# Kernel tuning notes

Hardware: AMD Instinct MI355X
Metric: run time of the kernel (lower is better)

Reference implementation:

```python
import jax, jax.numpy as jnp
import numpy as np
import math

B, C, H, W, P = 8, 64, 256, 256, 16


def _conv2d(x, w, groups=1):
    # x: [B,C,H,W], w: [O, I/groups, kh, kw], 'SAME' padding, stride 1
    return jax.lax.conv_general_dilated(
        x, w, window_strides=(1, 1), padding='SAME',
        dimension_numbers=('NCHW', 'OIHW', 'NCHW'),
        feature_group_count=groups)


def _bn(x, g, b, m, v, eps=1e-5):
    # inference-mode BatchNorm2d over channel dim
    inv = jax.lax.rsqrt(v + eps)
    return (x - m[None, :, None, None]) * (g * inv)[None, :, None, None] + b[None, :, None, None]


def _layernorm(x, g, b, eps=1e-5):
    mu = x.mean(-1, keepdims=True)
    var = ((x - mu) ** 2).mean(-1, keepdims=True)
    return (x - mu) * jax.lax.rsqrt(var + eps) * g + b


def setup_inputs() -> dict:
    key = jax.random.key(0)
    ks = jax.random.split(key, 16)
    feat_map = jax.random.normal(ks[0], (B, C, H, W), jnp.float32)
    query = jax.random.normal(ks[1], (B, P, C), jnp.float32)
    key_tokens = jax.random.normal(ks[2], (B, H * W, C), jnp.float32)
    s = 1.0 / math.sqrt(C)
    dw_w = jax.random.normal(ks[3], (C, 1, 3, 3), jnp.float32) * (1.0 / 3.0)
    pw_w = jax.random.normal(ks[4], (C, C, 1, 1), jnp.float32) * s
    bn1_g = jnp.ones((C,)); bn1_b = jnp.zeros((C,))
    bn1_m = jnp.zeros((C,)); bn1_v = jnp.ones((C,))
    bn2_g = jnp.ones((C,)); bn2_b = jnp.zeros((C,))
    bn2_m = jnp.zeros((C,)); bn2_v = jnp.ones((C,))
    aff_w = jax.random.normal(ks[5], (P, C), jnp.float32) * s
    loc_w1 = jax.random.normal(ks[6], (C, C), jnp.float32) * s
    loc_b1 = jnp.zeros((C,))
    loc_w2 = jax.random.normal(ks[7], (C, C), jnp.float32) * s
    loc_b2 = jnp.zeros((C,))
    glb_w1 = jax.random.normal(ks[8], (C, C), jnp.float32) * s
    glb_b1 = jnp.zeros((C,))
    glb_w2 = jax.random.normal(ks[9], (C, C), jnp.float32) * s
    glb_b2 = jnp.zeros((C,))
    ln_g = jnp.ones((C,)); ln_b = jnp.zeros((C,))
    topo_scale = jnp.float32(0.01)
    orient_scale = jnp.float32(0.01)
    angles = jnp.linspace(0.0, math.pi, P + 1)[:-1]
    proto_orient = jnp.stack([jnp.cos(2.0 * angles), jnp.sin(2.0 * angles)], axis=1).astype(jnp.float32)
    return dict(feat_map=feat_map, query=query, key_tokens=key_tokens,
                dw_w=dw_w, bn1_g=bn1_g, bn1_b=bn1_b, bn1_m=bn1_m, bn1_v=bn1_v,
                pw_w=pw_w, bn2_g=bn2_g, bn2_b=bn2_b, bn2_m=bn2_m, bn2_v=bn2_v,
                aff_w=aff_w,
                loc_w1=loc_w1, loc_b1=loc_b1, loc_w2=loc_w2, loc_b2=loc_b2,
                glb_w1=glb_w1, glb_b1=glb_b1, glb_w2=glb_w2, glb_b2=glb_b2,
                ln_g=ln_g, ln_b=ln_b, topo_scale=topo_scale, orient_scale=orient_scale,
                proto_orient=proto_orient)


def reference(feat_map, query, key_tokens,
              dw_w, bn1_g, bn1_b, bn1_m, bn1_v,
              pw_w, bn2_g, bn2_b, bn2_m, bn2_v,
              aff_w,
              loc_w1, loc_b1, loc_w2, loc_b2,
              glb_w1, glb_b1, glb_w2, glb_b2,
              ln_g, ln_b, topo_scale, orient_scale, proto_orient):
    b, c, h, w = feat_map.shape
    hw = h * w
    # conv_spatial: depthwise 3x3 -> BN -> ReLU -> 1x1 -> BN -> ReLU
    x = _conv2d(feat_map, dw_w, groups=c)
    x = jax.nn.relu(_bn(x, bn1_g, bn1_b, bn1_m, bn1_v))
    x = _conv2d(x, pw_w)
    x = jax.nn.relu(_bn(x, bn2_g, bn2_b, bn2_m, bn2_v))
    feat_conv = x.reshape(b, c, hw).transpose(0, 2, 1)  # [B, L, C]
    # Sobel edge magnitude on channel-mean map
    edge_input = feat_map.mean(axis=1, keepdims=True)  # [B,1,H,W]
    sob_x = jnp.array([[-1, 0, 1], [-2, 0, 2], [-1, 0, 1]], jnp.float32).reshape(1, 1, 3, 3)
    sob_y = jnp.array([[-1, -2, -1], [0, 0, 0], [1, 2, 1]], jnp.float32).reshape(1, 1, 3, 3)
    gx = _conv2d(edge_input, sob_x)
    gy = _conv2d(edge_input, sob_y)
    edge_strength = jnp.sqrt(gx * gx + gy * gy + 1e-6)  # [B,1,H,W]
    # standardized edge weight over tokens (unbiased std, matching torch.std)
    ew = edge_strength.reshape(b, hw, 1)
    ew_mean = ew.mean(axis=1, keepdims=True)
    ew_var = ((ew - ew_mean) ** 2).sum(axis=1, keepdims=True) / (hw - 1)
    edge_weight = (ew - ew_mean) / (jnp.sqrt(ew_var) + 1e-5)  # [B,L,1]
    # doubled-angle orientation encoding
    gx2 = gx * gx
    gy2 = gy * gy
    denom = gx2 + gy2 + 1e-6
    ori_x = (gx2 - gy2) / denom
    ori_y = 2.0 * gx * gy / denom
    orient_tokens = jnp.concatenate([ori_x, ori_y], axis=1).reshape(b, 2, hw).transpose(0, 2, 1)  # [B,L,2]
    edge_conf = edge_strength.reshape(b, hw, 1)
    edge_conf = edge_conf / (edge_conf.mean(axis=1, keepdims=True) + 1e-6)
    edge_conf = jnp.clip(edge_conf, 0.0, 3.0)
    # prototype orientation bias
    proto_dirs = proto_orient / jnp.maximum(
        jnp.linalg.norm(proto_orient, axis=-1, keepdims=True), 1e-12)
    orient_scores = jnp.einsum('blc,pc->blp', orient_tokens, proto_dirs)
    orient_bias = orient_scores * edge_conf  # [B,L,P]
    raw_affinity = jnp.einsum('blc,pc->blp', feat_conv, aff_w)
    affinity_logits = raw_affinity + topo_scale * edge_weight + orient_scale * orient_bias
    affinity = jax.nn.softmax(affinity_logits, axis=1)  # softmax over tokens L
    prototypes = jnp.einsum('blp,blc->bpc', affinity, key_tokens)  # [B,P,C]
    # Contextual Significance Weighting gate
    z = prototypes + query
    loc = jax.nn.relu(z @ loc_w1.T + loc_b1) @ loc_w2.T + loc_b2
    g_ctx = z.mean(axis=1, keepdims=True)
    glb = jax.nn.relu(g_ctx @ glb_w1.T + glb_b1) @ glb_w2.T + glb_b2
    attn_weights = jax.nn.sigmoid(loc + glb)
    out = _layernorm(query * attn_weights + query, ln_g, ln_b)
    return out
```

## Files before the change

### kernel.cpp

```cpp
#include <hip/hip_runtime.h>
#include <hip/hip_fp16.h>
#include <math.h>

#define HW     65536
#define WIDTH  256
#define HEIGHT 256

typedef __attribute__((ext_vector_type(8))) short bf16x8;
typedef __attribute__((ext_vector_type(4))) float f32x4;

__device__ __forceinline__ float relu_f(float x){ return x > 0.f ? x : 0.f; }
__device__ __forceinline__ unsigned int f2bf(float x){
    union { float f; unsigned int u; } v; v.f = x;
    unsigned int r = v.u + 0x7fffu + ((v.u >> 16) & 1u);
    return r >> 16;
}
__device__ __forceinline__ float bfbits2f(unsigned int lo16){
    union { unsigned int u; float f; } v; v.u = lo16 << 16; return v.f;
}
__device__ __forceinline__ float h2f(unsigned int bits16){
    __half h = *(__half*)&bits16; return __half2float(h);
}

__global__ void k_prep(const float* __restrict__ pw_w, const float* __restrict__ aff_w,
                       const float* __restrict__ g1, const float* __restrict__ b1,
                       const float* __restrict__ m1, const float* __restrict__ v1,
                       const float* __restrict__ g2, const float* __restrict__ b2,
                       const float* __restrict__ m2, const float* __restrict__ v2,
                       float* __restrict__ scsh, unsigned short* __restrict__ pwA,
                       unsigned short* __restrict__ affA){
    int t = threadIdx.x;
    for (int i = t; i < 4096; i += 256){
        int e = i & 7, l = (i >> 3) & 63, ks = (i >> 9) & 1, ct = i >> 10;
        int co = ct * 16 + (l & 15);
        int ci = ks * 32 + (l >> 4) * 8 + e;
        pwA[i] = (unsigned short)f2bf(pw_w[co * 64 + ci]);
    }
    for (int i = t; i < 1024; i += 256){
        int e = i & 7, l = (i >> 3) & 63, ks = i >> 9;
        int p = l & 15, k = ks * 32 + (l >> 4) * 8 + e;
        affA[i] = (unsigned short)f2bf(aff_w[p * 64 + k]);
    }
    if (t < 64){
        float s = g1[t] * rsqrtf(v1[t] + 1e-5f);
        scsh[t]       = s;
        scsh[64 + t]  = b1[t] - m1[t] * s;
        float s2 = g2[t] * rsqrtf(v2[t] + 1e-5f);
        scsh[128 + t] = s2;
        scsh[192 + t] = b2[t] - m2[t] * s2;
    }
}

__global__ __launch_bounds__(256, 4) void k_conv_aff(
    const float* __restrict__ feat, const float* __restrict__ dw_w,
    const float* __restrict__ scsh, const unsigned short* __restrict__ pwA,
    const unsigned short* __restrict__ affA,
    unsigned short* __restrict__ logitsH, float* __restrict__ ei)
{
    __shared__ unsigned short x1u[256 * 68];
    __shared__ float eibuf[4][256];
    int t = threadIdx.x;
    int lane = t & 63;
    int wu = __builtin_amdgcn_readfirstlane(t >> 6);
    int orig = blockIdx.x;
    int flat = (orig & 7) * 256 + (orig >> 3);
    int b = flat >> 8, h = flat & 255;

    const bf16x8* pwA8 = (const bf16x8*)pwA;
    bf16x8 apw0 = pwA8[(wu * 2 + 0) * 64 + lane];
    bf16x8 apw1 = pwA8[(wu * 2 + 1) * 64 + lane];
    const bf16x8* affA8 = (const bf16x8*)affA;
    bf16x8 aaf0 = affA8[lane];
    bf16x8 aaf1 = affA8[64 + lane];
    int lcol = lane & 15, pq = lane >> 4;
    int cb = wu * 16 + pq * 4;
    float4 sc2v = *(const float4*)(scsh + 128 + cb);
    float4 sh2v = *(const float4*)(scsh + 192 + cb);

    int px0 = lane * 4;
    const float* fb = feat + (size_t)b * 64 * HW;
    int hh0 = (h > 0) ? h - 1 : 0;
    int hh2 = (h < 255) ? h + 1 : 255;
    float rw0 = (h > 0) ? 1.f : 0.f;
    float rw2 = (h < 255) ? 1.f : 0.f;
    int   roff0 = hh0 * WIDTH, roff1 = h * WIDTH, roff2 = hh2 * WIDTH;
    float mx = 0.f, my = 0.f, mz = 0.f, mw = 0.f;
    int swz = ((lane >> 2) & 7) << 1;
    #pragma unroll
    for (int cp = 0; cp < 8; cp++){
        int ci0 = wu * 16 + cp * 2;
        int ci1 = ci0 + 1;
        const float* base0 = fb + (size_t)ci0 * HW + px0;
        const float* base1 = fb + (size_t)ci1 * HW + px0;
        float a00=0.f,a01=0.f,a02=0.f,a03=0.f, a10=0.f,a11=0.f,a12=0.f,a13=0.f;
        #pragma unroll
        for (int r = 0; r < 3; r++){
            int roff = (r == 0) ? roff0 : ((r == 1) ? roff1 : roff2);
            float rwf = (r == 0) ? rw0 : ((r == 1) ? 1.f : rw2);
            float4 v0 = *(const float4*)(base0 + roff);
            float4 v1 = *(const float4*)(base1 + roff);
            float w00 = dw_w[ci0*9 + r*3 + 0] * rwf;
            float w01 = dw_w[ci0*9 + r*3 + 1] * rwf;
            float w02 = dw_w[ci0*9 + r*3 + 2] * rwf;
            float w10 = dw_w[ci1*9 + r*3 + 0] * rwf;
            float w11 = dw_w[ci1*9 + r*3 + 1] * rwf;
            float w12 = dw_w[ci1*9 + r*3 + 2] * rwf;
            float lf0 = __shfl_up(v0.w, 1);  if (lane == 0)  lf0 = 0.f;
            float rt0 = __shfl_down(v0.x, 1); if (lane == 63) rt0 = 0.f;
            float lf1 = __shfl_up(v1.w, 1);  if (lane == 0)  lf1 = 0.f;
            float rt1 = __shfl_down(v1.x, 1); if (lane == 63) rt1 = 0.f;
            a00 += lf0*w00 + v0.x*w01 + v0.y*w02;
            a01 += v0.x*w00 + v0.y*w01 + v0.z*w02;
            a02 += v0.y*w00 + v0.z*w01 + v0.w*w02;
            a03 += v0.z*w00 + v0.w*w01 + rt0*w02;
            a10 += lf1*w10 + v1.x*w11 + v1.y*w12;
            a11 += v1.x*w10 + v1.y*w11 + v1.z*w12;
            a12 += v1.y*w10 + v1.z*w11 + v1.w*w12;
            a13 += v1.z*w10 + v1.w*w11 + rt1*w12;
            if (r == 1){
                mx += v0.x + v1.x; my += v0.y + v1.y;
                mz += v0.z + v1.z; mw += v0.w + v1.w;
            }
        }
        float s0 = scsh[ci0], o0 = scsh[64 + ci0];
        float s1 = scsh[ci1], o1 = scsh[64 + ci1];
        int dwi = ((wu * 8 + cp) ^ swz) * 2;
        unsigned int pk0 = f2bf(relu_f(fmaf(a00,s0,o0))) | (f2bf(relu_f(fmaf(a10,s1,o1))) << 16);
        unsigned int pk1 = f2bf(relu_f(fmaf(a01,s0,o0))) | (f2bf(relu_f(fmaf(a11,s1,o1))) << 16);
        unsigned int pk2 = f2bf(relu_f(fmaf(a02,s0,o0))) | (f2bf(relu_f(fmaf(a12,s1,o1))) << 16);
        unsigned int pk3 = f2bf(relu_f(fmaf(a03,s0,o0))) | (f2bf(relu_f(fmaf(a13,s1,o1))) << 16);
        *(unsigned int*)&x1u[(px0 + 0) * 68 + dwi] = pk0;
        *(unsigned int*)&x1u[(px0 + 1) * 68 + dwi] = pk1;
        *(unsigned int*)&x1u[(px0 + 2) * 68 + dwi] = pk2;
        *(unsigned int*)&x1u[(px0 + 3) * 68 + dwi] = pk3;
    }
    *(float4*)&eibuf[wu][px0] = make_float4(mx, my, mz, mw);
    __syncthreads();
    {
        float m = (eibuf[0][t] + eibuf[1][t]) + (eibuf[2][t] + eibuf[3][t]);
        ei[(size_t)b * HW + h * WIDTH + t] = m * (1.f / 64.f);
    }

    int k0d = pq * 4;
    #pragma unroll
    for (int half = 0; half < 2; half++){
        f32x4 accB[8];
        #pragma unroll
        for (int q = 0; q < 8; q++){
            int jt = half * 8 + q;
            int swzj = (jt & 7) << 1;
            const unsigned short* rowp = &x1u[(jt * 16 + lcol) * 68];
            union { bf16x8 v; uint2 u[2]; } b0, b1;
            b0.u[0] = *(const uint2*)&rowp[((k0d)          ^ swzj) * 2];
            b0.u[1] = *(const uint2*)&rowp[((k0d + 2)      ^ swzj) * 2];
            b1.u[0] = *(const uint2*)&rowp[((16 + k0d)     ^ swzj) * 2];
            b1.u[1] = *(const uint2*)&rowp[((16 + k0d + 2) ^ swzj) * 2];
            f32x4 acc = {0.f, 0.f, 0.f, 0.f};
            acc = __builtin_amdgcn_mfma_f32_16x16x32_bf16(apw0, b0.v, acc, 0, 0, 0);
            acc = __builtin_amdgcn_mfma_f32_16x16x32_bf16(apw1, b1.v, acc, 0, 0, 0);
            accB[q] = acc;
        }
        __syncthreads();
        #pragma unroll
        for (int q = 0; q < 8; q++){
            int jt = half * 8 + q;
            int swzj = (jt & 7) << 1;
            f32x4 acc = accB[q];
            unsigned int y0 = f2bf(relu_f(fmaf(acc[0], sc2v.x, sh2v.x)))
                            | (f2bf(relu_f(fmaf(acc[1], sc2v.y, sh2v.y))) << 16);
            unsigned int y1 = f2bf(relu_f(fmaf(acc[2], sc2v.z, sh2v.z)))
                            | (f2bf(relu_f(fmaf(acc[3], sc2v.w, sh2v.w))) << 16);
            int D = (wu * 8 + pq * 2) ^ swzj;
            *(uint2*)&x1u[(jt * 16 + lcol) * 68 + D * 2] = make_uint2(y0, y1);
        }
    }
    __syncthreads();

    int p0 = pq * 4;
    #pragma unroll
    for (int q = 0; q < 4; q++){
        int jt = wu * 4 + q;
        int swzj = (jt & 7) << 1;
        const unsigned short* rowp = &x1u[(jt * 16 + lcol) * 68];
        union { bf16x8 v; uint2 u[2]; } b0, b1;
        b0.u[0] = *(const uint2*)&rowp[((k0d)          ^ swzj) * 2];
        b0.u[1] = *(const uint2*)&rowp[((k0d + 2)      ^ swzj) * 2];
        b1.u[0] = *(const uint2*)&rowp[((16 + k0d)     ^ swzj) * 2];
        b1.u[1] = *(const uint2*)&rowp[((16 + k0d + 2) ^ swzj) * 2];
        f32x4 acc = {0.f, 0.f, 0.f, 0.f};
        acc = __builtin_amdgcn_mfma_f32_16x16x32_bf16(aaf0, b0.v, acc, 0, 0, 0);
        acc = __builtin_amdgcn_mfma_f32_16x16x32_bf16(aaf1, b1.v, acc, 0, 0, 0);
        int gx = h * WIDTH + jt * 16 + lcol;
        __half h0 = __float2half(acc[0]), h1v = __float2half(acc[1]);
        __half h2 = __float2half(acc[2]), h3v = __float2half(acc[3]);
        unsigned int u0 = (unsigned int)(*(unsigned short*)&h0)
                        | ((unsigned int)(*(unsigned short*)&h1v) << 16);
        unsigned int u1 = (unsigned int)(*(unsigned short*)&h2)
                        | ((unsigned int)(*(unsigned short*)&h3v) << 16);
        *(uint2*)&logitsH[((size_t)b * HW + gx) * 16 + p0] = make_uint2(u0, u1);
    }
}

__global__ __launch_bounds__(256) void k_sobel_stats(const float* __restrict__ ei,
                                                     float* __restrict__ part){
    int b = blockIdx.y, ch = blockIdx.x, t = threadIdx.x;
    const float* e = ei + (size_t)b * HW;
    float s1 = 0.f, s2 = 0.f;
    for (int i = 0; i < 4; i++){
        int l = ch * 1024 + i * 256 + t;
        int h = l >> 8, w = l & 255;
        float v[3][3];
        #pragma unroll
        for (int dh = -1; dh <= 1; dh++)
            #pragma unroll
            for (int dw = -1; dw <= 1; dw++){
                int hh = h + dh, ww = w + dw;
                v[dh+1][dw+1] = (hh >= 0 && hh < HEIGHT && ww >= 0 && ww < WIDTH)
                                ? e[hh * WIDTH + ww] : 0.f;
            }
        float gx = -v[0][0] + v[0][2] - 2.f*v[1][0] + 2.f*v[1][2] - v[2][0] + v[2][2];
        float gy = -v[0][0] - 2.f*v[0][1] - v[0][2] + v[2][0] + 2.f*v[2][1] + v[2][2];
        float esv = sqrtf(gx*gx + gy*gy + 1e-6f);
        s1 += esv; s2 += esv * esv;
    }
    __shared__ float r1[256], r2[256];
    r1[t] = s1; r2[t] = s2; __syncthreads();
    for (int s = 128; s > 0; s >>= 1){
        if (t < s){ r1[t] += r1[t+s]; r2[t] += r2[t+s]; }
        __syncthreads();
    }
    if (t == 0){ part[(b*64+ch)*2] = r1[0]; part[(b*64+ch)*2+1] = r2[0]; }
}

__global__ __launch_bounds__(256) void k_smproto(
    const unsigned short* __restrict__ logitsH, const float* __restrict__ ei,
    const float* __restrict__ part, const float* __restrict__ proto_orient,
    const float* __restrict__ topo_s, const float* __restrict__ orient_s,
    const float* __restrict__ key,
    float* __restrict__ smpart, float* __restrict__ ppart)
{
    int ch = blockIdx.x, b = blockIdx.y, t = threadIdx.x;
    __shared__ float eit[4][258];
    __shared__ float sstat[3];
    __shared__ float pdl[32];
    __shared__ float Ml[16];
    __shared__ float rm[4][16], rs[4][16];
    __shared__ unsigned int wlds[512][10];

    for (int i = t; i < 1024; i += 256){
        int r = i >> 8, c = i & 255;
        int row = 2 * ch - 1 + r;
        eit[r][c + 1] = (row >= 0 && row < 256) ? ei[(size_t)b * HW + row * 256 + c] : 0.f;
    }
    if (t >= 128 && t < 136){
        int q = t - 128;
        eit[q >> 1][(q & 1) * 257] = 0.f;
    }
    if (t < 64){
        float s1 = part[(b*64 + t)*2], s2 = part[(b*64 + t)*2 + 1];
        #pragma unroll
        for (int off = 32; off >= 1; off >>= 1){
            s1 += __shfl_xor(s1, off, 64);
            s2 += __shfl_xor(s2, off, 64);
        }
        if (t == 0){
            float mean = s1 / 65536.f;
            float var = (s2 - 65536.f * mean * mean) / 65535.f;
            var = var > 0.f ? var : 0.f;
            sstat[0] = mean;
            sstat[1] = 1.f / (sqrtf(var) + 1e-5f);
            sstat[2] = 1.f / (mean + 1e-6f);
        }
    } else if (t >= 64 && t < 80){
        int p = t - 64;
        float nx = proto_orient[p*2], ny = proto_orient[p*2+1];
        float n = sqrtf(nx*nx + ny*ny);
        n = n > 1e-12f ? n : 1e-12f;
        pdl[p*2] = nx / n; pdl[p*2+1] = ny / n;
    }
    __syncthreads();
    float mean = sstat[0], rstd = sstat[1], cinv = sstat[2];
    float topo = topo_s[0], orient = orient_s[0];

    float m[16], s[16];
    #pragma unroll
    for (int p = 0; p < 16; p++){ m[p] = -1e30f; s[p] = 0.f; }
    uint4 pkA0, pkA1, pkB0, pkB1;
    {
        size_t gl0 = ((size_t)b * HW + ch * 512 + t) * 16;
        size_t gl1 = ((size_t)b * HW + ch * 512 + 256 + t) * 16;
        pkA0 = *(const uint4*)&logitsH[gl0];
        pkA1 = *(const uint4*)&logitsH[gl0 + 8];
        pkB0 = *(const uint4*)&logitsH[gl1];
        pkB1 = *(const uint4*)&logitsH[gl1 + 8];
    }
    float ewv[2], oxv[2], oyv[2];
    #pragma unroll
    for (int i = 0; i < 2; i++){
        int hl = i + 1, w = t;
        float vmm = eit[hl-1][w], vm0 = eit[hl-1][w+1], vmp = eit[hl-1][w+2];
        float v0m = eit[hl][w],                          v0p = eit[hl][w+2];
        float vpm = eit[hl+1][w], vp0 = eit[hl+1][w+1], vpp = eit[hl+1][w+2];
        float gx = vmp - vmm + 2.f*(v0p - v0m) + vpp - vpm;
        float gy = vpm + 2.f*vp0 + vpp - vmm - 2.f*vm0 - vmp;
        float denom = gx*gx + gy*gy + 1e-6f;
        float esv = sqrtf(denom);
        float cf = fminf(fmaxf(esv * cinv, 0.f), 3.f);
        ewv[i] = (esv - mean) * rstd;
        oxv[i] = ((gx*gx - gy*gy) / denom) * cf;
        oyv[i] = (2.f * gx * gy / denom) * cf;
        const uint4& q0 = (i == 0) ? pkA0 : pkB0;
        const uint4& q1 = (i == 0) ? pkA1 : pkB1;
        unsigned int wv[8] = {q0.x, q0.y, q0.z, q0.w, q1.x, q1.y, q1.z, q1.w};
        #pragma unroll
        for (int p = 0; p < 16; p++){
            unsigned int bits = (p & 1) ? (wv[p >> 1] >> 16) : (wv[p >> 1] & 0xffffu);
            float x = h2f(bits) + topo * ewv[i]
                    + orient * (oxv[i]*pdl[p*2] + oyv[i]*pdl[p*2+1]);
            float mn = fmaxf(m[p], x);
            s[p] = s[p] * __expf(m[p] - mn) + __expf(x - mn);
            m[p] = mn;
        }
    }
    #pragma unroll
    for (int p = 0; p < 16; p++){
        #pragma unroll
        for (int off = 32; off >= 1; off >>= 1){
            float m2 = __shfl_xor(m[p], off, 64);
            float s2v = __shfl_xor(s[p], off, 64);
            float mn = fmaxf(m[p], m2);
            s[p] = s[p] * __expf(m[p] - mn) + s2v * __expf(m2 - mn);
            m[p] = mn;
        }
    }
    int wid = t >> 6;
    if ((t & 63) == 0){
        #pragma unroll
        for (int p = 0; p < 16; p++){ rm[wid][p] = m[p]; rs[wid][p] = s[p]; }
    }
    __syncthreads();
    if (t < 16){
        float M = -1e30f, S = 0.f;
        #pragma unroll
        for (int w2 = 0; w2 < 4; w2++){
            float mw = rm[w2][t], sw2 = rs[w2][t];
            float mn = fmaxf(M, mw);
            S = S * __expf(M - mn) + sw2 * __expf(mw - mn);
            M = mn;
        }
        smpart[((b*16 + t)*128 + ch)*2]     = M;
        smpart[((b*16 + t)*128 + ch)*2 + 1] = S;
        Ml[t] = M;
    }
    __syncthreads();
    float Mloc[16];
    #pragma unroll
    for (int p = 0; p < 16; p++) Mloc[p] = Ml[p];

    #pragma unroll
    for (int i = 0; i < 2; i++){
        int tok = i * 256 + t;
        const uint4& q0 = (i == 0) ? pkA0 : pkB0;
        const uint4& q1 = (i == 0) ? pkA1 : pkB1;
        unsigned int wv[8] = {q0.x, q0.y, q0.z, q0.w, q1.x, q1.y, q1.z, q1.w};
        #pragma unroll
        for (int p2 = 0; p2 < 8; p2++){
            int pa = p2*2, pb2 = p2*2 + 1;
            float xa = h2f(wv[p2] & 0xffffu) + topo*ewv[i]
                     + orient*(oxv[i]*pdl[pa*2]  + oyv[i]*pdl[pa*2+1]);
            float xb = h2f(wv[p2] >> 16) + topo*ewv[i]
                     + orient*(oxv[i]*pdl[pb2*2] + oyv[i]*pdl[pb2*2+1]);
            wlds[tok][p2] = f2bf(__expf(xa - Mloc[pa])) | (f2bf(__expf(xb - Mloc[pb2])) << 16);
        }
    }
    __syncthreads();

    int w = t >> 6, lane = t & 63, cg = lane & 15, pq = lane >> 4;
    const float4* kp = (const float4*)key + ((size_t)b * HW + ch * 512 + w * 128) * 16 + cg;
    float acc[4][4];
    #pragma unroll
    for (int j = 0; j < 4; j++)
        #pragma unroll
        for (int i = 0; i < 4; i++) acc[j][i] = 0.f;
    for (int blk = 0; blk < 16; blk++){
        float4 kv[8]; uint2 wv2[8];
        #pragma unroll
        for (int j = 0; j < 8; j++){
            kv[j]  = kp[(blk*8 + j) * 16];
            wv2[j] = *(const uint2*)&wlds[w*128 + blk*8 + j][pq*2];
        }
        #pragma unroll
        for (int j = 0; j < 8; j++){
            float w0 = bfbits2f(wv2[j].x & 0xffffu);
            float w1 = bfbits2f(wv2[j].x >> 16);
            float w2 = bfbits2f(wv2[j].y & 0xffffu);
            float w3 = bfbits2f(wv2[j].y >> 16);
            float4 kv4 = kv[j];
            acc[0][0] = fmaf(w0, kv4.x, acc[0][0]); acc[0][1] = fmaf(w0, kv4.y, acc[0][1]);
            acc[0][2] = fmaf(w0, kv4.z, acc[0][2]); acc[0][3] = fmaf(w0, kv4.w, acc[0][3]);
            acc[1][0] = fmaf(w1, kv4.x, acc[1][0]); acc[1][1] = fmaf(w1, kv4.y, acc[1][1]);
            acc[1][2] = fmaf(w1, kv4.z, acc[1][2]); acc[1][3] = fmaf(w1, kv4.w, acc[1][3]);
            acc[2][0] = fmaf(w2, kv4.x, acc[2][0]); acc[2][1] = fmaf(w2, kv4.y, acc[2][1]);
            acc[2][2] = fmaf(w2, kv4.z, acc[2][2]); acc[2][3] = fmaf(w2, kv4.w, acc[2][3]);
            acc[3][0] = fmaf(w3, kv4.x, acc[3][0]); acc[3][1] = fmaf(w3, kv4.y, acc[3][1]);
            acc[3][2] = fmaf(w3, kv4.z, acc[3][2]); acc[3][3] = fmaf(w3, kv4.w, acc[3][3]);
        }
    }
    __syncthreads();
    float (*red)[16][68] = (float (*)[16][68])wlds;
    #pragma unroll
    for (int j = 0; j < 4; j++)
        *(float4*)&red[w][pq*4 + j][cg*4] =
            make_float4(acc[j][0], acc[j][1], acc[j][2], acc[j][3]);
    __syncthreads();
    size_t obase = ((size_t)(b * 128 + ch)) * 1024;
    for (int idx = t; idx < 1024; idx += 256){
        int p = idx >> 6, c = idx & 63;
        ppart[obase + idx] = red[0][p][c] + red[1][p][c] + red[2][p][c] + red[3][p][c];
    }
}

__global__ __launch_bounds__(256) void k_reduce(
    const float* __restrict__ smpart, const float* __restrict__ ppart,
    float* __restrict__ proto)
{
    int p = blockIdx.x, b = blockIdx.y, t = threadIdx.x;
    __shared__ float arr[128], flv[128], partial[4][64];
    float Mt = -1e30f, St = 0.f;
    if (t < 128){
        Mt = smpart[((b*16 + p)*128 + t)*2];
        St = smpart[((b*16 + p)*128 + t)*2 + 1];
        arr[t] = Mt;
    }
    __syncthreads();
    for (int s = 64; s > 0; s >>= 1){
        if (t < s) arr[t] = fmaxf(arr[t], arr[t + s]);
        __syncthreads();
    }
    float M = arr[0];
    __syncthreads();
    if (t < 128) arr[t] = St * __expf(Mt - M);
    __syncthreads();
    for (int s = 64; s > 0; s >>= 1){
        if (t < s) arr[t] += arr[t + s];
        __syncthreads();
    }
    float Stot = arr[0];
    __syncthreads();
    if (t < 128) flv[t] = __expf(Mt - M) / Stot;
    __syncthreads();
    int c = t & 63, half = t >> 6;
    float acc = 0.f;
    #pragma unroll 8
    for (int j = 0; j < 32; j++){
        int ch = half * 32 + j;
        acc += flv[ch] * ppart[((size_t)(b * 128 + ch)) * 1024 + p * 64 + c];
    }
    partial[half][c] = acc;
    __syncthreads();
    if (t < 64)
        proto[b * 1024 + p * 64 + t] =
            (partial[0][t] + partial[1][t]) + (partial[2][t] + partial[3][t]);
}

__global__ __launch_bounds__(256) void k_gate(
    const float* __restrict__ proto, const float* __restrict__ query,
    const float* __restrict__ w1, const float* __restrict__ bb1,
    const float* __restrict__ w2, const float* __restrict__ bb2,
    const float* __restrict__ gw1, const float* __restrict__ gb1,
    const float* __restrict__ gw2, const float* __restrict__ gb2,
    const float* __restrict__ lng, const float* __restrict__ lnb,
    float* __restrict__ out)
{
    __shared__ float z[16][64], h1[16][64], loc[16][64], g[64], hg[64], glb[64];
    int b = blockIdx.x, t = threadIdx.x;
    for (int idx = t; idx < 1024; idx += 256)
        z[idx >> 6][idx & 63] = proto[b * 1024 + idx] + query[b * 1024 + idx];
    __syncthreads();
    for (int idx = t; idx < 1024; idx += 256){
        int p = idx >> 6, j = idx & 63;
        float acc = bb1[j];
        for (int i = 0; i < 64; i++) acc += z[p][i] * w1[j * 64 + i];
        h1[p][j] = relu_f(acc);
    }
    if (t < 64){
        float sg = 0.f;
        for (int p = 0; p < 16; p++) sg += z[p][t];
        g[t] = sg * (1.f / 16.f);
    }
    __syncthreads();
    for (int idx = t; idx < 1024; idx += 256){
        int p = idx >> 6, k = idx & 63;
        float acc = bb2[k];
        for (int j = 0; j < 64; j++) acc += h1[p][j] * w2[k * 64 + j];
        loc[p][k] = acc;
    }
    if (t < 64){
        float acc = gb1[t];
        for (int i = 0; i < 64; i++) acc += g[i] * gw1[t * 64 + i];
        hg[t] = relu_f(acc);
    }
    __syncthreads();
    if (t < 64){
        float acc = gb2[t];
        for (int j = 0; j < 64; j++) acc += hg[j] * gw2[t * 64 + j];
        glb[t] = acc;
    }
    __syncthreads();
    for (int idx = t; idx < 1024; idx += 256){
        int p = idx >> 6, c = idx & 63;
        float a = loc[p][c] + glb[c];
        float sg = 1.f / (1.f + expf(-a));
        float q = query[b * 1024 + idx];
        h1[p][c] = q * sg + q;
    }
    __syncthreads();
    if (t < 16){
        int p = t;
        float mu = 0.f;
        for (int c = 0; c < 64; c++) mu += h1[p][c];
        mu *= (1.f / 64.f);
        float var = 0.f;
        for (int c = 0; c < 64; c++){ float d = h1[p][c] - mu; var += d * d; }
        var *= (1.f / 64.f);
        float rstd = rsqrtf(var + 1e-5f);
        for (int c = 0; c < 64; c++)
            out[b * 1024 + p * 64 + c] = (h1[p][c] - mu) * rstd * lng[c] + lnb[c];
    }
}

extern "C" void kernel_launch(void* const* d_in, const int* in_sizes, int n_in,
                              void* d_out, int out_size, void* d_ws, size_t ws_size,
                              hipStream_t stream){
    (void)in_sizes; (void)n_in; (void)out_size; (void)ws_size;
    const float* feat   = (const float*)d_in[0];
    const float* query  = (const float*)d_in[1];
    const float* key    = (const float*)d_in[2];
    const float* dw_w   = (const float*)d_in[3];
    const float* bn1_g  = (const float*)d_in[4];
    const float* bn1_b  = (const float*)d_in[5];
    const float* bn1_m  = (const float*)d_in[6];
    const float* bn1_v  = (const float*)d_in[7];
    const float* pw_w   = (const float*)d_in[8];
    const float* bn2_g  = (const float*)d_in[9];
    const float* bn2_b  = (const float*)d_in[10];
    const float* bn2_m  = (const float*)d_in[11];
    const float* bn2_v  = (const float*)d_in[12];
    const float* aff_w  = (const float*)d_in[13];
    const float* loc_w1 = (const float*)d_in[14];
    const float* loc_b1 = (const float*)d_in[15];
    const float* loc_w2 = (const float*)d_in[16];
    const float* loc_b2 = (const float*)d_in[17];
    const float* glb_w1 = (const float*)d_in[18];
    const float* glb_b1 = (const float*)d_in[19];
    const float* glb_w2 = (const float*)d_in[20];
    const float* glb_b2 = (const float*)d_in[21];
    const float* ln_g   = (const float*)d_in[22];
    const float* ln_b   = (const float*)d_in[23];
    const float* topo   = (const float*)d_in[24];
    const float* orient = (const float*)d_in[25];
    const float* proto_orient = (const float*)d_in[26];
    float* out = (float*)d_out;
    float* ws  = (float*)d_ws;

    float* ei      = ws;
    unsigned short* logitsH = (unsigned short*)(ws + 1048576);
    float* ppart   = ws + 5242880;
    float* k3part  = ws + 6291456;
    float* smpart  = ws + 6292480;
    float* proto   = ws + 6325248;
    float* scsh    = ws + 6333440;
    unsigned short* pwA  = (unsigned short*)(ws + 6333696);
    unsigned short* affA = (unsigned short*)(ws + 6335744);

    k_prep<<<1, 256, 0, stream>>>(pw_w, aff_w, bn1_g, bn1_b, bn1_m, bn1_v,
                                  bn2_g, bn2_b, bn2_m, bn2_v, scsh, pwA, affA);
    k_conv_aff<<<2048, 256, 0, stream>>>(feat, dw_w, scsh, pwA, affA, logitsH, ei);
    k_sobel_stats<<<dim3(64, 8), 256, 0, stream>>>(ei, k3part);
    k_smproto<<<dim3(128, 8), 256, 0, stream>>>(logitsH, ei, k3part, proto_orient,
                                                topo, orient, key, smpart, ppart);
    k_reduce<<<dim3(16, 8), 256, 0, stream>>>(smpart, ppart, proto);
    k_gate<<<8, 256, 0, stream>>>(proto, query, loc_w1, loc_b1, loc_w2, loc_b2,
                                  glb_w1, glb_b1, glb_w2, glb_b2, ln_g, ln_b, out);
}
```

Baseline: 130.9 us.

## Vectorize Sobel stats with row-wise shuffles and restructure prototype accumulation

The Sobel statistics kernel now has each wave handle one image row: it loads float4 rows, fetches neighbours through lane shuffles, and reduces with wave-level shuffles instead of a shared-memory tree. In the prototype accumulation, each lane now loads each key token once and accumulates all 16 prototypes, followed by a cross-lane shuffle reduction. Previously every key element was reloaded by four lane groups. This removes redundant global loads but raises register pressure to 64 accumulators per thread and adds shuffle reduction overhead.

```diff
diff --git a/kernel.cpp b/kernel.cpp
--- a/kernel.cpp
+++ b/kernel.cpp
@@ -203,33 +203,49 @@
 
 __global__ __launch_bounds__(256) void k_sobel_stats(const float* __restrict__ ei,
                                                      float* __restrict__ part){
-    int b = blockIdx.y, ch = blockIdx.x, t = threadIdx.x;
+    int ch = blockIdx.x, b = blockIdx.y, t = threadIdx.x;
+    int lane = t & 63, w = t >> 6;
+    int h = ch * 4 + w;
+    int px0 = lane * 4;
     const float* e = ei + (size_t)b * HW;
+    int hh0 = (h > 0) ? h - 1 : 0;
+    int hh2 = (h < 255) ? h + 1 : 255;
+    float rw0 = (h > 0) ? 1.f : 0.f;
+    float rw2 = (h < 255) ? 1.f : 0.f;
+    float4 v0 = *(const float4*)(e + hh0 * WIDTH + px0);
+    float4 v1 = *(const float4*)(e + h   * WIDTH + px0);
+    float4 v2 = *(const float4*)(e + hh2 * WIDTH + px0);
+    v0.x *= rw0; v0.y *= rw0; v0.z *= rw0; v0.w *= rw0;
+    v2.x *= rw2; v2.y *= rw2; v2.z *= rw2; v2.w *= rw2;
+    float l0 = __shfl_up(v0.w, 1);   if (lane == 0)  l0 = 0.f;
+    float r0 = __shfl_down(v0.x, 1); if (lane == 63) r0 = 0.f;
+    float l1 = __shfl_up(v1.w, 1);   if (lane == 0)  l1 = 0.f;
+    float r1 = __shfl_down(v1.x, 1); if (lane == 63) r1 = 0.f;
+    float l2 = __shfl_up(v2.w, 1);   if (lane == 0)  l2 = 0.f;
+    float r2 = __shfl_down(v2.x, 1); if (lane == 63) r2 = 0.f;
+    float t0[6]  = {l0, v0.x, v0.y, v0.z, v0.w, r0};
+    float m1a[6] = {l1, v1.x, v1.y, v1.z, v1.w, r1};
+    float b2a[6] = {l2, v2.x, v2.y, v2.z, v2.w, r2};
     float s1 = 0.f, s2 = 0.f;
-    for (int i = 0; i < 4; i++){
-        int l = ch * 1024 + i * 256 + t;
-        int h = l >> 8, w = l & 255;
-        float v[3][3];
-        #pragma unroll
-        for (int dh = -1; dh <= 1; dh++)
-            #pragma unroll
-            for (int dw = -1; dw <= 1; dw++){
-                int hh = h + dh, ww = w + dw;
-                v[dh+1][dw+1] = (hh >= 0 && hh < HEIGHT && ww >= 0 && ww < WIDTH)
-                                ? e[hh * WIDTH + ww] : 0.f;
-            }
-        float gx = -v[0][0] + v[0][2] - 2.f*v[1][0] + 2.f*v[1][2] - v[2][0] + v[2][2];
-        float gy = -v[0][0] - 2.f*v[0][1] - v[0][2] + v[2][0] + 2.f*v[2][1] + v[2][2];
+    #pragma unroll
+    for (int j = 0; j < 4; j++){
+        float gx = (t0[j+2] - t0[j]) + 2.f*(m1a[j+2] - m1a[j]) + (b2a[j+2] - b2a[j]);
+        float gy = (b2a[j] + 2.f*b2a[j+1] + b2a[j+2]) - (t0[j] + 2.f*t0[j+1] + t0[j+2]);
         float esv = sqrtf(gx*gx + gy*gy + 1e-6f);
         s1 += esv; s2 += esv * esv;
     }
-    __shared__ float r1[256], r2[256];
-    r1[t] = s1; r2[t] = s2; __syncthreads();
-    for (int s = 128; s > 0; s >>= 1){
-        if (t < s){ r1[t] += r1[t+s]; r2[t] += r2[t+s]; }
-        __syncthreads();
-    }
-    if (t == 0){ part[(b*64+ch)*2] = r1[0]; part[(b*64+ch)*2+1] = r2[0]; }
+    #pragma unroll
+    for (int off = 32; off >= 1; off >>= 1){
+        s1 += __shfl_xor(s1, off, 64);
+        s2 += __shfl_xor(s2, off, 64);
+    }
+    __shared__ float rs1[4], rs2[4];
+    if (lane == 0){ rs1[w] = s1; rs2[w] = s2; }
+    __syncthreads();
+    if (t == 0)
+        part[(b*64+ch)*2]     = (rs1[0] + rs1[1]) + (rs1[2] + rs1[3]);
+    if (t == 1)
+        part[(b*64+ch)*2 + 1] = (rs2[0] + rs2[1]) + (rs2[2] + rs2[3]);
 }
 
 __global__ __launch_bounds__(256) void k_smproto(
@@ -375,43 +391,53 @@
     }
     __syncthreads();
 
-    int w = t >> 6, lane = t & 63, cg = lane & 15, pq = lane >> 4;
-    const float4* kp = (const float4*)key + ((size_t)b * HW + ch * 512 + w * 128) * 16 + cg;
-    float acc[4][4];
-    #pragma unroll
-    for (int j = 0; j < 4; j++)
-        #pragma unroll
-        for (int i = 0; i < 4; i++) acc[j][i] = 0.f;
-    for (int blk = 0; blk < 16; blk++){
-        float4 kv[8]; uint2 wv2[8];
-        #pragma unroll
-        for (int j = 0; j < 8; j++){
-            kv[j]  = kp[(blk*8 + j) * 16];
-            wv2[j] = *(const uint2*)&wlds[w*128 + blk*8 + j][pq*2];
-        }
-        #pragma unroll
-        for (int j = 0; j < 8; j++){
-            float w0 = bfbits2f(wv2[j].x & 0xffffu);
-            float w1 = bfbits2f(wv2[j].x >> 16);
-            float w2 = bfbits2f(wv2[j].y & 0xffffu);
-            float w3 = bfbits2f(wv2[j].y >> 16);
-            float4 kv4 = kv[j];
-            acc[0][0] = fmaf(w0, kv4.x, acc[0][0]); acc[0][1] = fmaf(w0, kv4.y, acc[0][1]);
-            acc[0][2] = fmaf(w0, kv4.z, acc[0][2]); acc[0][3] = fmaf(w0, kv4.w, acc[0][3]);
-            acc[1][0] = fmaf(w1, kv4.x, acc[1][0]); acc[1][1] = fmaf(w1, kv4.y, acc[1][1]);
-            acc[1][2] = fmaf(w1, kv4.z, acc[1][2]); acc[1][3] = fmaf(w1, kv4.w, acc[1][3]);
-            acc[2][0] = fmaf(w2, kv4.x, acc[2][0]); acc[2][1] = fmaf(w2, kv4.y, acc[2][1]);
-            acc[2][2] = fmaf(w2, kv4.z, acc[2][2]); acc[2][3] = fmaf(w2, kv4.w, acc[2][3]);
-            acc[3][0] = fmaf(w3, kv4.x, acc[3][0]); acc[3][1] = fmaf(w3, kv4.y, acc[3][1]);
-            acc[3][2] = fmaf(w3, kv4.z, acc[3][2]); acc[3][3] = fmaf(w3, kv4.w, acc[3][3]);
-        }
-    }
+    int w = t >> 6, lane = t & 63, cg = lane & 15, g = lane >> 4;
+    const float4* kp = (const float4*)key + ((size_t)b * HW + ch * 512 + w * 128) * 16;
+    float acc[16][4];
+    #pragma unroll
+    for (int p = 0; p < 16; p++)
+        #pragma unroll
+        for (int i = 0; i < 4; i++) acc[p][i] = 0.f;
+    #pragma unroll 4
+    for (int blk = 0; blk < 32; blk++){
+        int tok = blk * 4 + g;
+        float4 kv = kp[tok * 16 + cg];
+        const unsigned int* wp = &wlds[w * 128 + tok][0];
+        uint2 q0 = *(const uint2*)&wp[0];
+        uint2 q1 = *(const uint2*)&wp[2];
+        uint2 q2 = *(const uint2*)&wp[4];
+        uint2 q3 = *(const uint2*)&wp[6];
+        unsigned int ww[8] = {q0.x, q0.y, q1.x, q1.y, q2.x, q2.y, q3.x, q3.y};
+        #pragma unroll
+        for (int p2 = 0; p2 < 8; p2++){
+            float wa = bfbits2f(ww[p2] & 0xffffu);
+            float wb = bfbits2f(ww[p2] >> 16);
+            int pa = 2*p2, pb2 = 2*p2 + 1;
+            acc[pa][0] = fmaf(wa, kv.x, acc[pa][0]);
+            acc[pa][1] = fmaf(wa, kv.y, acc[pa][1]);
+            acc[pa][2] = fmaf(wa, kv.z, acc[pa][2]);
+            acc[pa][3] = fmaf(wa, kv.w, acc[pa][3]);
+            acc[pb2][0] = fmaf(wb, kv.x, acc[pb2][0]);
+            acc[pb2][1] = fmaf(wb, kv.y, acc[pb2][1]);
+            acc[pb2][2] = fmaf(wb, kv.z, acc[pb2][2]);
+            acc[pb2][3] = fmaf(wb, kv.w, acc[pb2][3]);
+        }
+    }
+    #pragma unroll
+    for (int p = 0; p < 16; p++)
+        #pragma unroll
+        for (int i = 0; i < 4; i++){
+            acc[p][i] += __shfl_xor(acc[p][i], 16, 64);
+            acc[p][i] += __shfl_xor(acc[p][i], 32, 64);
+        }
     __syncthreads();
     float (*red)[16][68] = (float (*)[16][68])wlds;
-    #pragma unroll
-    for (int j = 0; j < 4; j++)
-        *(float4*)&red[w][pq*4 + j][cg*4] =
-            make_float4(acc[j][0], acc[j][1], acc[j][2], acc[j][3]);
+    if (g == 0){
+        #pragma unroll
+        for (int p = 0; p < 16; p++)
+            *(float4*)&red[w][p][cg*4] =
+                make_float4(acc[p][0], acc[p][1], acc[p][2], acc[p][3]);
+    }
     __syncthreads();
     size_t obase = ((size_t)(b * 128 + ch)) * 1024;
     for (int idx = t; idx < 1024; idx += 256){
```

Measured after the change: 128.2 us. -2.0%, faster.
